# Performance work log

Hardware: AMD Instinct MI355X
Metric: run time of the kernel (lower is better)

The kernel has to match this reference:

```python
import jax, jax.numpy as jnp
import numpy as np

N, E = 50000, 800000
D_IN, D_HID, D_OUT = 128, 256, 128


def setup_inputs() -> dict:
    key = jax.random.key(0)
    k = jax.random.split(key, 7)
    x = jax.random.normal(k[0], (N, D_IN), dtype=jnp.float32)
    edge_src = jax.random.randint(k[1], (E,), 0, N, dtype=jnp.int32)
    edge_dst = jax.random.randint(k[2], (E,), 0, N, dtype=jnp.int32)
    s1 = 1.0 / np.sqrt(2 * D_IN)
    s2 = 1.0 / np.sqrt(2 * D_HID)
    W1 = jax.random.uniform(k[3], (2 * D_IN, D_HID), jnp.float32, -s1, s1)
    b1 = jax.random.uniform(k[4], (D_HID,), jnp.float32, -s1, s1)
    W2 = jax.random.uniform(k[5], (2 * D_HID, D_OUT), jnp.float32, -s2, s2)
    b2 = jax.random.uniform(k[6], (D_OUT,), jnp.float32, -s2, s2)
    return {"x": x, "edge_src": edge_src, "edge_dst": edge_dst,
            "W1": W1, "b1": b1, "W2": W2, "b2": b2}


def _sage_layer(h, edge_src, edge_dst, W, b, inv_deg):
    # mean-pool neighbor features: gather [E, D] then segment-sum to [N, D]
    msgs = h[edge_src]
    agg = jax.ops.segment_sum(msgs, edge_dst, num_segments=h.shape[0]) * inv_deg
    y = jnp.concatenate([h, agg], axis=1)  # [N, 2D]
    return y @ W + b


def reference(x, edge_src, edge_dst, W1, b1, W2, b2):
    n = x.shape[0]
    deg = jax.ops.segment_sum(jnp.ones_like(edge_dst, dtype=x.dtype), edge_dst,
                              num_segments=n)
    inv_deg = (1.0 / jnp.maximum(deg, 1.0))[:, None]  # isolated nodes -> zeros
    h = _sage_layer(x, edge_src, edge_dst, W1, b1, inv_deg)
    h = jax.nn.relu(h)
    # dropout is identity in eval mode
    h = _sage_layer(h, edge_src, edge_dst, W2, b2, inv_deg)
    return jax.nn.log_softmax(h, axis=1)
```

## Files before the change

### kernel.cpp

```cpp
#include <hip/hip_runtime.h>
#include <cstdint>
#include <cstddef>

typedef __attribute__((ext_vector_type(8))) short bf16x8;
typedef __attribute__((ext_vector_type(4))) float f32x4;
typedef __attribute__((ext_vector_type(2))) float f32x2;

__device__ inline short bf16_rne(float f) {
  unsigned u = __builtin_bit_cast(unsigned, f);
  u += 0x7fff + ((u >> 16) & 1);
  return (short)(u >> 16);
}

__device__ inline float bf16lo(unsigned v) { return __builtin_bit_cast(float, v << 16); }
__device__ inline float bf16hi(unsigned v) { return __builtin_bit_cast(float, v & 0xffff0000u); }

__device__ inline unsigned pack2(float a, float b) {
  return ((unsigned)(unsigned short)bf16_rne(a)) | (((unsigned)(unsigned short)bf16_rne(b)) << 16);
}

__device__ inline void async_copy16(const void* g, void* l) {
  __builtin_amdgcn_global_load_lds((const __attribute__((address_space(1))) void*)g,
                                   (__attribute__((address_space(3))) void*)l, 16, 0, 0);
}


__global__ __launch_bounds__(256) void bucket_hist(const int* __restrict__ dst, int E, int EPB,
                                                   int* __restrict__ histT, int SB, int NB) {
  __shared__ int h[512];
  int tid = threadIdx.x;
  for (int t = tid; t < NB; t += 256) h[t] = 0;
  __syncthreads();
  int start = blockIdx.x * EPB, end = min(E, start + EPB);
  for (int i = start + tid; i < end; i += 256) atomicAdd(&h[((unsigned)dst[i]) >> 7], 1);
  __syncthreads();
  for (int t = tid; t < NB; t += 256) histT[t * SB + blockIdx.x] = h[t];
}

__global__ __launch_bounds__(1024) void scan1_kernel(const int* __restrict__ in,
                                                     int* __restrict__ outx,
                                                     int* __restrict__ part, int n) {
  __shared__ int buf[1024];
  int tid = threadIdx.x;
  int i = blockIdx.x * 1024 + tid;
  int v = (i < n) ? in[i] : 0;
  buf[tid] = v;
  __syncthreads();
  #pragma unroll
  for (int off = 1; off < 1024; off <<= 1) {
    int t = (tid >= off) ? buf[tid - off] : 0;
    __syncthreads();
    buf[tid] += t;
    __syncthreads();
  }
  if (i < n) outx[i] = buf[tid] - v;
  if (tid == 1023) part[blockIdx.x] = buf[1023];
}

__global__ __launch_bounds__(1024) void scan2_kernel(int* __restrict__ part, int B) {
  __shared__ int buf[1024];
  int tid = threadIdx.x;
  int v = (tid < B) ? part[tid] : 0;
  buf[tid] = v;
  __syncthreads();
  #pragma unroll
  for (int off = 1; off < 1024; off <<= 1) {
    int t = (tid >= off) ? buf[tid - off] : 0;
    __syncthreads();
    buf[tid] += t;
    __syncthreads();
  }
  if (tid < B) part[tid] = buf[tid] - v;
}

__global__ __launch_bounds__(256) void bucket_scatter(const int* __restrict__ src,
                                                      const int* __restrict__ dst, int E, int EPB,
                                                      const int* __restrict__ excl,
                                                      const int* __restrict__ part, int SB, int NB,
                                                      unsigned* __restrict__ bedge) {
  __shared__ int cur[512];
  int tid = threadIdx.x;
  for (int t = tid; t < NB; t += 256) cur[t] = excl[t * SB + blockIdx.x] + part[t];
  __syncthreads();
  int start = blockIdx.x * EPB, end = min(E, start + EPB);
  for (int i = start + tid; i < end; i += 256) {
    unsigned d = (unsigned)dst[i];
    int p = atomicAdd(&cur[d >> 7], 1);
    bedge[p] = ((d & 127u) << 24) | (unsigned)src[i];
  }
}

__global__ __launch_bounds__(256) void build_csr(const unsigned* __restrict__ bedge,
                                                 const int* __restrict__ excl,
                                                 const int* __restrict__ part, int SB, int NB,
                                                 int N, int E,
                                                 int* __restrict__ offsets,
                                                 float* __restrict__ inv_deg,
                                                 int* __restrict__ ssrc) {
  __shared__ int buf[128];
  int b = blockIdx.x, tid = threadIdx.x;
  int estart = excl[b * SB] + part[b];
  int eend = (b == NB - 1) ? E : (excl[(b + 1) * SB] + part[b + 1]);
  if (tid < 128) buf[tid] = 0;
  __syncthreads();
  for (int i = estart + tid; i < eend; i += 256) atomicAdd(&buf[bedge[i] >> 24], 1);
  __syncthreads();
  int cnt = (tid < 128) ? buf[tid] : 0;
  #pragma unroll
  for (int off = 1; off < 128; off <<= 1) {
    int t = (tid >= off && tid < 128) ? buf[tid - off] : 0;
    __syncthreads();
    if (tid < 128) buf[tid] += t;
    __syncthreads();
  }
  if (tid < 128) {
    int excl_l = buf[tid] - cnt;
    int node = (b << 7) + tid;
    if (node < N) {
      offsets[node] = estart + excl_l;
      inv_deg[node] = 1.0f / fmaxf((float)cnt, 1.0f);
    }
    if (node == N) offsets[N] = E;
    buf[tid] = estart + excl_l;
  }
  __syncthreads();
  for (int i = estart + tid; i < eend; i += 256) {
    unsigned e2 = bedge[i];
    int p = atomicAdd(&buf[e2 >> 24], 1);
    ssrc[p] = (int)(e2 & 0xFFFFFFu);
  }
}

__global__ __launch_bounds__(256) void prep_kernel(const float* __restrict__ W1,
                                                   const float* __restrict__ W2,
                                                   const float* __restrict__ b2,
                                                   const float* __restrict__ x,
                                                   short* __restrict__ B1p,
                                                   short* __restrict__ B2p,
                                                   float* __restrict__ bias2,
                                                   unsigned* __restrict__ A1u,
                                                   unsigned* __restrict__ xf8, int nquads) {
  int b = blockIdx.x;
  if (b < 512) {
    int mode = b >> 8;
    int idx = (b & 255) * 256 + threadIdx.x;
    int j = idx & 7;
    int L = (idx >> 3) & 63;
    int nt = (idx >> 9) & 15;
    int kb = idx >> 13;
    int k = kb * 32 + (L >> 4) * 8 + j;
    int n = nt * 16 + (L & 15);
    if (mode == 0) {
      B1p[idx] = bf16_rne(W1[(size_t)k * 256 + n]);
    } else {
      float v = (n < 128) ? W2[(size_t)k * 128 + n] : W2[(size_t)(256 + k) * 128 + (n - 128)];
      B2p[idx] = bf16_rne(v);
    }
  } else if (b == 512) {
    int j = threadIdx.x;
    bias2[j] = (j < 128) ? b2[j] : 0.0f;
  } else {
    int idx = (b - 513) * 256 + threadIdx.x;
    if (idx < nquads) {
      int n = idx >> 5, q = idx & 31;
      float4 v = ((const float4*)x)[idx];
      ((uint2*)A1u)[(size_t)n * 64 + q] = make_uint2(pack2(v.x, v.y), pack2(v.z, v.w));
      int pk = __builtin_amdgcn_cvt_pk_fp8_f32(v.x, v.y, 0, false);
      pk = __builtin_amdgcn_cvt_pk_fp8_f32(v.z, v.w, pk, true);
      xf8[(size_t)n * 32 + q] = (unsigned)pk;
    }
  }
}


__global__ __launch_bounds__(256) void agg1_kernel(const uint2* __restrict__ X8,
                                                   const int* __restrict__ offsets,
                                                   const int* __restrict__ ssrc,
                                                   const float* __restrict__ inv_deg,
                                                   uint4* __restrict__ A1q, int N) {
  int node = blockIdx.x * 4 + (threadIdx.x >> 6);
  if (node >= N) return;
  int lane = threadIdx.x & 63;
  int g = lane >> 4;
  int l = lane & 15;
  int s = offsets[node], e = offsets[node + 1];
  float a0=0.f,a1=0.f,a2=0.f,a3=0.f,a4=0.f,a5=0.f,a6=0.f,a7=0.f;
  int i = s;
  for (; i + 8 <= e; i += 8) {
    int sA = ssrc[i + g], sB = ssrc[i + 4 + g];
    uint2 u = X8[((size_t)(unsigned)sA << 4) + l];
    uint2 v = X8[((size_t)(unsigned)sB << 4) + l];
    f32x2 p, q;
    p = __builtin_amdgcn_cvt_pk_f32_fp8(u.x, false); q = __builtin_amdgcn_cvt_pk_f32_fp8(u.x, true);
    a0 += p[0]; a1 += p[1]; a2 += q[0]; a3 += q[1];
    p = __builtin_amdgcn_cvt_pk_f32_fp8(u.y, false); q = __builtin_amdgcn_cvt_pk_f32_fp8(u.y, true);
    a4 += p[0]; a5 += p[1]; a6 += q[0]; a7 += q[1];
    p = __builtin_amdgcn_cvt_pk_f32_fp8(v.x, false); q = __builtin_amdgcn_cvt_pk_f32_fp8(v.x, true);
    a0 += p[0]; a1 += p[1]; a2 += q[0]; a3 += q[1];
    p = __builtin_amdgcn_cvt_pk_f32_fp8(v.y, false); q = __builtin_amdgcn_cvt_pk_f32_fp8(v.y, true);
    a4 += p[0]; a5 += p[1]; a6 += q[0]; a7 += q[1];
  }
  for (; i < e; i += 4) {
    if (g < e - i) {
      uint2 u = X8[((size_t)(unsigned)ssrc[i + g] << 4) + l];
      f32x2 p, q;
      p = __builtin_amdgcn_cvt_pk_f32_fp8(u.x, false); q = __builtin_amdgcn_cvt_pk_f32_fp8(u.x, true);
      a0 += p[0]; a1 += p[1]; a2 += q[0]; a3 += q[1];
      p = __builtin_amdgcn_cvt_pk_f32_fp8(u.y, false); q = __builtin_amdgcn_cvt_pk_f32_fp8(u.y, true);
      a4 += p[0]; a5 += p[1]; a6 += q[0]; a7 += q[1];
    }
  }
  a0 += __shfl_xor(a0,16,64); a0 += __shfl_xor(a0,32,64);
  a1 += __shfl_xor(a1,16,64); a1 += __shfl_xor(a1,32,64);
  a2 += __shfl_xor(a2,16,64); a2 += __shfl_xor(a2,32,64);
  a3 += __shfl_xor(a3,16,64); a3 += __shfl_xor(a3,32,64);
  a4 += __shfl_xor(a4,16,64); a4 += __shfl_xor(a4,32,64);
  a5 += __shfl_xor(a5,16,64); a5 += __shfl_xor(a5,32,64);
  a6 += __shfl_xor(a6,16,64); a6 += __shfl_xor(a6,32,64);
  a7 += __shfl_xor(a7,16,64); a7 += __shfl_xor(a7,32,64);
  if (g == 0) {
    float id = inv_deg[node];
    A1q[((size_t)node << 5) + 16 + l] =
        make_uint4(pack2(a0 * id, a1 * id), pack2(a2 * id, a3 * id),
                   pack2(a4 * id, a5 * id), pack2(a6 * id, a7 * id));
  }
}

__global__ __launch_bounds__(256) void gemm_mfma(const short* __restrict__ A,
                                                 const short* __restrict__ Bp,
                                                 const float* __restrict__ bias,
                                                 void* __restrict__ out0,
                                                 void* __restrict__ out1,
                                                 int M_pad, int mode) {
  __shared__ __align__(16) short As[4096];
  __shared__ __align__(16) short Bs[4096];
  int tid = threadIdx.x;
  int w = tid >> 6;
  int lane = tid & 63;
  int wr = w >> 1;
  int wc = w & 1;
  int bm = blockIdx.x * 128;
  int bn = blockIdx.y * 128;

  f32x4 acc[4][4];
  #pragma unroll
  for (int i = 0; i < 4; ++i)
    #pragma unroll
    for (int j = 0; j < 4; ++j) acc[i][j] = (f32x4)(0.0f);

  for (int kb = 0; kb < 8; ++kb) {
    #pragma unroll
    for (int q = 0; q < 2; ++q) {
      int f = q * 4 + w;
      int row = bm + f * 16 + (lane & 15);
      const short* g = A + (size_t)row * 256 + kb * 32 + (lane >> 4) * 8;
      async_copy16(g, &As[f * 512]);
    }
    #pragma unroll
    for (int q = 0; q < 2; ++q) {
      int f = q * 4 + w;
      const short* g = Bp + ((size_t)(kb * 16 + (bn >> 4) + f) * 64 + lane) * 8;
      async_copy16(g, &Bs[f * 512]);
    }
    __syncthreads();

    bf16x8 af[4], bfr[4];
    #pragma unroll
    for (int i = 0; i < 4; ++i)
      af[i] = *(const bf16x8*)&As[(wr * 4 + i) * 512 + lane * 8];
    #pragma unroll
    for (int j = 0; j < 4; ++j)
      bfr[j] = *(const bf16x8*)&Bs[(wc * 4 + j) * 512 + lane * 8];

    #pragma unroll
    for (int i = 0; i < 4; ++i)
      #pragma unroll
      for (int j = 0; j < 4; ++j)
        acc[i][j] = __builtin_amdgcn_mfma_f32_16x16x32_bf16(af[i], bfr[j], acc[i][j], 0, 0, 0);
    __syncthreads();
  }

  int crow0 = (lane >> 4) * 4;
  int ccol = lane & 15;
  #pragma unroll
  for (int i = 0; i < 4; ++i) {
    #pragma unroll
    for (int j = 0; j < 4; ++j) {
      int col_loc = wc * 64 + j * 16 + ccol;
      int col = bn + col_loc;
      #pragma unroll
      for (int r = 0; r < 4; ++r) {
        int row = bm + wr * 64 + i * 16 + crow0 + r;
        float v = acc[i][j][r] + bias[col];
        if (mode == 0) {
          v = fmaxf(v, 0.0f);
          ((short*)out0)[(size_t)row * 256 + col] = bf16_rne(v);
        } else if (blockIdx.y == 0) {
          ((short*)out0)[(size_t)row * 128 + col_loc] = bf16_rne(v);
        } else {
          int pk = __builtin_amdgcn_cvt_pk_fp8_f32(v, v, 0, false);
          ((unsigned char*)out1)[(size_t)row * 128 + col_loc] = (unsigned char)(pk & 0xff);
        }
      }
    }
  }
}

__global__ __launch_bounds__(256) void final_kernel(const uint4* __restrict__ utopq,
                                                    const uint2* __restrict__ T2,
                                                    const int* __restrict__ offsets,
                                                    const int* __restrict__ ssrc,
                                                    const float* __restrict__ inv_deg,
                                                    float4* __restrict__ out4, int N) {
  int node = blockIdx.x * 4 + (threadIdx.x >> 6);
  if (node >= N) return;
  int lane = threadIdx.x & 63;
  int g = lane >> 4;
  int l = lane & 15;
  int s = offsets[node], e = offsets[node + 1];
  float a0=0.f,a1=0.f,a2=0.f,a3=0.f,a4=0.f,a5=0.f,a6=0.f,a7=0.f;
  int i = s;
  for (; i + 8 <= e; i += 8) {
    int sA = ssrc[i + g], sB = ssrc[i + 4 + g];
    uint2 u = T2[((size_t)(unsigned)sA << 4) + l];
    uint2 v = T2[((size_t)(unsigned)sB << 4) + l];
    f32x2 p, q;
    p = __builtin_amdgcn_cvt_pk_f32_fp8(u.x, false); q = __builtin_amdgcn_cvt_pk_f32_fp8(u.x, true);
    a0 += p[0]; a1 += p[1]; a2 += q[0]; a3 += q[1];
    p = __builtin_amdgcn_cvt_pk_f32_fp8(u.y, false); q = __builtin_amdgcn_cvt_pk_f32_fp8(u.y, true);
    a4 += p[0]; a5 += p[1]; a6 += q[0]; a7 += q[1];
    p = __builtin_amdgcn_cvt_pk_f32_fp8(v.x, false); q = __builtin_amdgcn_cvt_pk_f32_fp8(v.x, true);
    a0 += p[0]; a1 += p[1]; a2 += q[0]; a3 += q[1];
    p = __builtin_amdgcn_cvt_pk_f32_fp8(v.y, false); q = __builtin_amdgcn_cvt_pk_f32_fp8(v.y, true);
    a4 += p[0]; a5 += p[1]; a6 += q[0]; a7 += q[1];
  }
  for (; i < e; i += 4) {
    if (g < e - i) {
      uint2 u = T2[((size_t)(unsigned)ssrc[i + g] << 4) + l];
      f32x2 p, q;
      p = __builtin_amdgcn_cvt_pk_f32_fp8(u.x, false); q = __builtin_amdgcn_cvt_pk_f32_fp8(u.x, true);
      a0 += p[0]; a1 += p[1]; a2 += q[0]; a3 += q[1];
      p = __builtin_amdgcn_cvt_pk_f32_fp8(u.y, false); q = __builtin_amdgcn_cvt_pk_f32_fp8(u.y, true);
      a4 += p[0]; a5 += p[1]; a6 += q[0]; a7 += q[1];
    }
  }
  a0 += __shfl_xor(a0,16,64); a0 += __shfl_xor(a0,32,64);
  a1 += __shfl_xor(a1,16,64); a1 += __shfl_xor(a1,32,64);
  a2 += __shfl_xor(a2,16,64); a2 += __shfl_xor(a2,32,64);
  a3 += __shfl_xor(a3,16,64); a3 += __shfl_xor(a3,32,64);
  a4 += __shfl_xor(a4,16,64); a4 += __shfl_xor(a4,32,64);
  a5 += __shfl_xor(a5,16,64); a5 += __shfl_xor(a5,32,64);
  a6 += __shfl_xor(a6,16,64); a6 += __shfl_xor(a6,32,64);
  a7 += __shfl_xor(a7,16,64); a7 += __shfl_xor(a7,32,64);
  if (g == 0) {
    float id = inv_deg[node];
    uint4 U = utopq[((size_t)node << 4) + l];
    float v0 = bf16lo(U.x) + a0 * id;
    float v1 = bf16hi(U.x) + a1 * id;
    float v2 = bf16lo(U.y) + a2 * id;
    float v3 = bf16hi(U.y) + a3 * id;
    float v4 = bf16lo(U.z) + a4 * id;
    float v5 = bf16hi(U.z) + a5 * id;
    float v6 = bf16lo(U.w) + a6 * id;
    float v7 = bf16hi(U.w) + a7 * id;
    float m = fmaxf(fmaxf(fmaxf(v0, v1), fmaxf(v2, v3)), fmaxf(fmaxf(v4, v5), fmaxf(v6, v7)));
    #pragma unroll
    for (int off = 1; off < 16; off <<= 1) m = fmaxf(m, __shfl_xor(m, off, 16));
    float su = expf(v0 - m) + expf(v1 - m) + expf(v2 - m) + expf(v3 - m) +
               expf(v4 - m) + expf(v5 - m) + expf(v6 - m) + expf(v7 - m);
    #pragma unroll
    for (int off = 1; off < 16; off <<= 1) su += __shfl_xor(su, off, 16);
    float ls = m + logf(su);
    out4[((size_t)node << 5) + l * 2]     = make_float4(v0 - ls, v1 - ls, v2 - ls, v3 - ls);
    out4[((size_t)node << 5) + l * 2 + 1] = make_float4(v4 - ls, v5 - ls, v6 - ls, v7 - ls);
  }
}

extern "C" void kernel_launch(void* const* d_in, const int* in_sizes, int n_in,
                              void* d_out, int out_size, void* d_ws, size_t ws_size,
                              hipStream_t stream) {
  const float* x        = (const float*)d_in[0];
  const int*   edge_src = (const int*)d_in[1];
  const int*   edge_dst = (const int*)d_in[2];
  const float* W1       = (const float*)d_in[3];
  const float* b1       = (const float*)d_in[4];
  const float* W2       = (const float*)d_in[5];
  const float* b2       = (const float*)d_in[6];
  float* out = (float*)d_out;

  const int D_IN = 128;
  const int N = in_sizes[0] / D_IN;
  const int E = in_sizes[1];
  const int M_pad = ((N + 127) / 128) * 128;

  const int SB = 1024;
  const int EPB = (E + SB - 1) / SB;
  const int NB = (N + 127) >> 7;
  const int M = NB * SB;
  const int sbl = (M + 1023) / 1024;

  char* ws = (char*)d_ws;
  size_t p = 0;
  auto take = [&](size_t bytes) -> size_t {
    size_t r = p;
    p += (bytes + 255) & ~(size_t)255;
    return r;
  };
  size_t histT_off = take((size_t)M * 4);
  size_t excl_off  = take((size_t)(M + 1) * 4);
  size_t part_off  = take((size_t)1024 * 4);
  size_t bedge_off = take((size_t)E * 4);
  size_t offs_off  = take((size_t)(N + 1) * 4);
  size_t inv_off   = take((size_t)N * 4);
  size_t ssrc_off  = take((size_t)E * 4);
  size_t A1_off    = take((size_t)M_pad * 256 * 2);
  size_t xf8_off   = take((size_t)M_pad * 128);
  size_t h_off     = take((size_t)M_pad * 256 * 2);
  size_t B1p_off   = take((size_t)256 * 256 * 2);
  size_t B2p_off   = take((size_t)256 * 256 * 2);
  size_t bias2_off = take((size_t)256 * 4);
  size_t utop_off  = take((size_t)M_pad * 128 * 2);
  size_t t2_off    = take((size_t)M_pad * 128);
  (void)ws_size;

  int*   histT   = (int*)(ws + histT_off);
  int*   excl    = (int*)(ws + excl_off);
  int*   part    = (int*)(ws + part_off);
  unsigned* bedge = (unsigned*)(ws + bedge_off);
  int*   offsets = (int*)(ws + offs_off);
  float* inv_deg = (float*)(ws + inv_off);
  int*   ssrc    = (int*)(ws + ssrc_off);
  unsigned* A1u  = (unsigned*)(ws + A1_off);
  unsigned* xf8  = (unsigned*)(ws + xf8_off);
  short* h       = (short*)(ws + h_off);
  short* B1p     = (short*)(ws + B1p_off);
  short* B2p     = (short*)(ws + B2p_off);
  float* bias2   = (float*)(ws + bias2_off);
  short* utop    = (short*)(ws + utop_off);
  unsigned char* t2f8 = (unsigned char*)(ws + t2_off);

  bucket_hist<<<SB, 256, 0, stream>>>(edge_dst, E, EPB, histT, SB, NB);
  scan1_kernel<<<sbl, 1024, 0, stream>>>(histT, excl, part, M);
  scan2_kernel<<<1, 1024, 0, stream>>>(part, sbl);
  bucket_scatter<<<SB, 256, 0, stream>>>(edge_src, edge_dst, E, EPB, excl, part, SB, NB, bedge);
  build_csr<<<NB, 256, 0, stream>>>(bedge, excl, part, SB, NB, N, E, offsets, inv_deg, ssrc);

  {
    int nquads = N * 32;
    int grid = 513 + (nquads + 255) / 256;
    prep_kernel<<<grid, 256, 0, stream>>>(W1, W2, b2, x, B1p, B2p, bias2, A1u, xf8, nquads);
  }

  agg1_kernel<<<(N + 3) / 4, 256, 0, stream>>>((const uint2*)xf8, offsets, ssrc, inv_deg,
                                               (uint4*)A1u, N);
  {
    dim3 grid(M_pad / 128, 2);
    gemm_mfma<<<grid, 256, 0, stream>>>((const short*)A1u, B1p, b1, h, nullptr, M_pad, 0);
  }
  {
    dim3 grid(M_pad / 128, 2);
    gemm_mfma<<<grid, 256, 0, stream>>>(h, B2p, bias2, utop, t2f8, M_pad, 1);
  }
  final_kernel<<<(N + 3) / 4, 256, 0, stream>>>((const uint4*)utop, (const uint2*)t2f8,
                                                offsets, ssrc, inv_deg, (float4*)out, N);
}
```

Before: 236.9 us.

## Fuse histogram into prep kernel, halve sort blocks, unroll gathers by sixteen

Merges the bucket histogram and the weight/feature prep work into one launch, so the independent work shares a grid and one kernel launch goes away. The sort block count drops from 1024 to 512, and the scan uses 512-thread blocks with one block per bucket. Both neighbour-aggregation kernels now gather 16 edges per iteration instead of 8, keeping more loads in flight. Fewer sort blocks means less parallelism in the scatter stage, and the deeper unroll sends more edges to the tail loop for low-degree nodes.

Result: faster. 228.6 us (-3.5%).

```diff
diff --git a/kernel.cpp b/kernel.cpp
--- a/kernel.cpp
+++ b/kernel.cpp
@@ -25,36 +25,77 @@
 }
 
 
-__global__ __launch_bounds__(256) void bucket_hist(const int* __restrict__ dst, int E, int EPB,
-                                                   int* __restrict__ histT, int SB, int NB) {
+__global__ __launch_bounds__(256) void prep_kernel(const int* __restrict__ dst, int E, int EPB,
+                                                   int* __restrict__ histT, int SB, int NB,
+                                                   const float* __restrict__ W1,
+                                                   const float* __restrict__ W2,
+                                                   const float* __restrict__ b2,
+                                                   const float* __restrict__ x,
+                                                   short* __restrict__ B1p,
+                                                   short* __restrict__ B2p,
+                                                   float* __restrict__ bias2,
+                                                   unsigned* __restrict__ A1u,
+                                                   unsigned* __restrict__ xf8, int nquads) {
   __shared__ int h[512];
+  int b = blockIdx.x;
   int tid = threadIdx.x;
-  for (int t = tid; t < NB; t += 256) h[t] = 0;
-  __syncthreads();
-  int start = blockIdx.x * EPB, end = min(E, start + EPB);
-  for (int i = start + tid; i < end; i += 256) atomicAdd(&h[((unsigned)dst[i]) >> 7], 1);
-  __syncthreads();
-  for (int t = tid; t < NB; t += 256) histT[t * SB + blockIdx.x] = h[t];
-}
-
-__global__ __launch_bounds__(1024) void scan1_kernel(const int* __restrict__ in,
-                                                     int* __restrict__ outx,
-                                                     int* __restrict__ part, int n) {
-  __shared__ int buf[1024];
+  if (b < SB) {
+    for (int t = tid; t < NB; t += 256) h[t] = 0;
+    __syncthreads();
+    int start = b * EPB, end = min(E, start + EPB);
+    for (int i = start + tid; i < end; i += 256) atomicAdd(&h[((unsigned)dst[i]) >> 7], 1);
+    __syncthreads();
+    for (int t = tid; t < NB; t += 256) histT[t * SB + b] = h[t];
+  } else if (b < SB + 512) {
+    int bb = b - SB;
+    int mode = bb >> 8;
+    int idx = (bb & 255) * 256 + tid;
+    int j = idx & 7;
+    int L = (idx >> 3) & 63;
+    int nt = (idx >> 9) & 15;
+    int kb = idx >> 13;
+    int k = kb * 32 + (L >> 4) * 8 + j;
+    int n = nt * 16 + (L & 15);
+    if (mode == 0) {
+      B1p[idx] = bf16_rne(W1[(size_t)k * 256 + n]);
+    } else {
+      float v = (n < 128) ? W2[(size_t)k * 128 + n] : W2[(size_t)(256 + k) * 128 + (n - 128)];
+      B2p[idx] = bf16_rne(v);
+    }
+  } else if (b == SB + 512) {
+    int j = tid;
+    bias2[j] = (j < 128) ? b2[j] : 0.0f;
+  } else {
+    int idx = (b - SB - 513) * 256 + tid;
+    if (idx < nquads) {
+      int n = idx >> 5, q = idx & 31;
+      float4 v = ((const float4*)x)[idx];
+      ((uint2*)A1u)[(size_t)n * 64 + q] = make_uint2(pack2(v.x, v.y), pack2(v.z, v.w));
+      int pk = __builtin_amdgcn_cvt_pk_fp8_f32(v.x, v.y, 0, false);
+      pk = __builtin_amdgcn_cvt_pk_fp8_f32(v.z, v.w, pk, true);
+      xf8[(size_t)n * 32 + q] = (unsigned)pk;
+    }
+  }
+}
+
+__global__ __launch_bounds__(512) void scan1_kernel(const int* __restrict__ in,
+                                                    int* __restrict__ outx,
+                                                    int* __restrict__ part, int n) {
+  __shared__ int buf[512];
   int tid = threadIdx.x;
-  int i = blockIdx.x * 1024 + tid;
+  int i = blockIdx.x * 512 + tid;
   int v = (i < n) ? in[i] : 0;
   buf[tid] = v;
   __syncthreads();
   #pragma unroll
-  for (int off = 1; off < 1024; off <<= 1) {
+  for (int off = 1; off < 512; off <<= 1) {
     int t = (tid >= off) ? buf[tid - off] : 0;
     __syncthreads();
     buf[tid] += t;
     __syncthreads();
   }
   if (i < n) outx[i] = buf[tid] - v;
-  if (tid == 1023) part[blockIdx.x] = buf[1023];
+  if (tid == 511) part[blockIdx.x] = buf[511];
 }
 
 __global__ __launch_bounds__(1024) void scan2_kernel(int* __restrict__ part, int B) {
@@ -131,47 +172,16 @@
   }
 }
 
-__global__ __launch_bounds__(256) void prep_kernel(const float* __restrict__ W1,
-                                                   const float* __restrict__ W2,
-                                                   const float* __restrict__ b2,
-                                                   const float* __restrict__ x,
-                                                   short* __restrict__ B1p,
-                                                   short* __restrict__ B2p,
-                                                   float* __restrict__ bias2,
-                                                   unsigned* __restrict__ A1u,
-                                                   unsigned* __restrict__ xf8, int nquads) {
-  int b = blockIdx.x;
-  if (b < 512) {
-    int mode = b >> 8;
-    int idx = (b & 255) * 256 + threadIdx.x;
-    int j = idx & 7;
-    int L = (idx >> 3) & 63;
-    int nt = (idx >> 9) & 15;
-    int kb = idx >> 13;
-    int k = kb * 32 + (L >> 4) * 8 + j;
-    int n = nt * 16 + (L & 15);
-    if (mode == 0) {
-      B1p[idx] = bf16_rne(W1[(size_t)k * 256 + n]);
-    } else {
-      float v = (n < 128) ? W2[(size_t)k * 128 + n] : W2[(size_t)(256 + k) * 128 + (n - 128)];
-      B2p[idx] = bf16_rne(v);
-    }
-  } else if (b == 512) {
-    int j = threadIdx.x;
-    bias2[j] = (j < 128) ? b2[j] : 0.0f;
-  } else {
-    int idx = (b - 513) * 256 + threadIdx.x;
-    if (idx < nquads) {
-      int n = idx >> 5, q = idx & 31;
-      float4 v = ((const float4*)x)[idx];
-      ((uint2*)A1u)[(size_t)n * 64 + q] = make_uint2(pack2(v.x, v.y), pack2(v.z, v.w));
-      int pk = __builtin_amdgcn_cvt_pk_fp8_f32(v.x, v.y, 0, false);
-      pk = __builtin_amdgcn_cvt_pk_fp8_f32(v.z, v.w, pk, true);
-      xf8[(size_t)n * 32 + q] = (unsigned)pk;
-    }
-  }
-}
-
+#define CVT8(U, A0, A1, A2, A3, A4, A5, A6, A7)                                        \
+  {                                                                                    \
+    f32x2 p_, q_;                                                                      \
+    p_ = __builtin_amdgcn_cvt_pk_f32_fp8((U).x, false);                                \
+    q_ = __builtin_amdgcn_cvt_pk_f32_fp8((U).x, true);                                 \
+    A0 += p_[0]; A1 += p_[1]; A2 += q_[0]; A3 += q_[1];                                \
+    p_ = __builtin_amdgcn_cvt_pk_f32_fp8((U).y, false);                                \
+    q_ = __builtin_amdgcn_cvt_pk_f32_fp8((U).y, true);                                 \
+    A4 += p_[0]; A5 += p_[1]; A6 += q_[0]; A7 += q_[1];                                \
+  }
 
 __global__ __launch_bounds__(256) void agg1_kernel(const uint2* __restrict__ X8,
                                                    const int* __restrict__ offsets,
@@ -186,28 +196,22 @@
   int s = offsets[node], e = offsets[node + 1];
   float a0=0.f,a1=0.f,a2=0.f,a3=0.f,a4=0.f,a5=0.f,a6=0.f,a7=0.f;
   int i = s;
-  for (; i + 8 <= e; i += 8) {
+  for (; i + 16 <= e; i += 16) {
     int sA = ssrc[i + g], sB = ssrc[i + 4 + g];
+    int sC = ssrc[i + 8 + g], sD = ssrc[i + 12 + g];
     uint2 u = X8[((size_t)(unsigned)sA << 4) + l];
     uint2 v = X8[((size_t)(unsigned)sB << 4) + l];
-    f32x2 p, q;
-    p = __builtin_amdgcn_cvt_pk_f32_fp8(u.x, false); q = __builtin_amdgcn_cvt_pk_f32_fp8(u.x, true);
-    a0 += p[0]; a1 += p[1]; a2 += q[0]; a3 += q[1];
-    p = __builtin_amdgcn_cvt_pk_f32_fp8(u.y, false); q = __builtin_amdgcn_cvt_pk_f32_fp8(u.y, true);
-    a4 += p[0]; a5 += p[1]; a6 += q[0]; a7 += q[1];
-    p = __builtin_amdgcn_cvt_pk_f32_fp8(v.x, false); q = __builtin_amdgcn_cvt_pk_f32_fp8(v.x, true);
-    a0 += p[0]; a1 += p[1]; a2 += q[0]; a3 += q[1];
-    p = __builtin_amdgcn_cvt_pk_f32_fp8(v.y, false); q = __builtin_amdgcn_cvt_pk_f32_fp8(v.y, true);
-    a4 += p[0]; a5 += p[1]; a6 += q[0]; a7 += q[1];
+    uint2 w = X8[((size_t)(unsigned)sC << 4) + l];
+    uint2 z = X8[((size_t)(unsigned)sD << 4) + l];
+    CVT8(u, a0,a1,a2,a3,a4,a5,a6,a7);
+    CVT8(v, a0,a1,a2,a3,a4,a5,a6,a7);
+    CVT8(w, a0,a1,a2,a3,a4,a5,a6,a7);
+    CVT8(z, a0,a1,a2,a3,a4,a5,a6,a7);
   }
   for (; i < e; i += 4) {
     if (g < e - i) {
       uint2 u = X8[((size_t)(unsigned)ssrc[i + g] << 4) + l];
-      f32x2 p, q;
-      p = __builtin_amdgcn_cvt_pk_f32_fp8(u.x, false); q = __builtin_amdgcn_cvt_pk_f32_fp8(u.x, true);
-      a0 += p[0]; a1 += p[1]; a2 += q[0]; a3 += q[1];
-      p = __builtin_amdgcn_cvt_pk_f32_fp8(u.y, false); q = __builtin_amdgcn_cvt_pk_f32_fp8(u.y, true);
-      a4 += p[0]; a5 += p[1]; a6 += q[0]; a7 += q[1];
+      CVT8(u, a0,a1,a2,a3,a4,a5,a6,a7);
     }
   }
   a0 += __shfl_xor(a0,16,64); a0 += __shfl_xor(a0,32,64);
@@ -320,28 +324,22 @@
   int s = offsets[node], e = offsets[node + 1];
   float a0=0.f,a1=0.f,a2=0.f,a3=0.f,a4=0.f,a5=0.f,a6=0.f,a7=0.f;
   int i = s;
-  for (; i + 8 <= e; i += 8) {
+  for (; i + 16 <= e; i += 16) {
     int sA = ssrc[i + g], sB = ssrc[i + 4 + g];
+    int sC = ssrc[i + 8 + g], sD = ssrc[i + 12 + g];
     uint2 u = T2[((size_t)(unsigned)sA << 4) + l];
     uint2 v = T2[((size_t)(unsigned)sB << 4) + l];
-    f32x2 p, q;
-    p = __builtin_amdgcn_cvt_pk_f32_fp8(u.x, false); q = __builtin_amdgcn_cvt_pk_f32_fp8(u.x, true);
-    a0 += p[0]; a1 += p[1]; a2 += q[0]; a3 += q[1];
-    p = __builtin_amdgcn_cvt_pk_f32_fp8(u.y, false); q = __builtin_amdgcn_cvt_pk_f32_fp8(u.y, true);
-    a4 += p[0]; a5 += p[1]; a6 += q[0]; a7 += q[1];
-    p = __builtin_amdgcn_cvt_pk_f32_fp8(v.x, false); q = __builtin_amdgcn_cvt_pk_f32_fp8(v.x, true);
-    a0 += p[0]; a1 += p[1]; a2 += q[0]; a3 += q[1];
-    p = __builtin_amdgcn_cvt_pk_f32_fp8(v.y, false); q = __builtin_amdgcn_cvt_pk_f32_fp8(v.y, true);
-    a4 += p[0]; a5 += p[1]; a6 += q[0]; a7 += q[1];
+    uint2 w = T2[((size_t)(unsigned)sC << 4) + l];
+    uint2 z = T2[((size_t)(unsigned)sD << 4) + l];
+    CVT8(u, a0,a1,a2,a3,a4,a5,a6,a7);
+    CVT8(v, a0,a1,a2,a3,a4,a5,a6,a7);
+    CVT8(w, a0,a1,a2,a3,a4,a5,a6,a7);
+    CVT8(z, a0,a1,a2,a3,a4,a5,a6,a7);
   }
   for (; i < e; i += 4) {
     if (g < e - i) {
       uint2 u = T2[((size_t)(unsigned)ssrc[i + g] << 4) + l];
-      f32x2 p, q;
-      p = __builtin_amdgcn_cvt_pk_f32_fp8(u.x, false); q = __builtin_amdgcn_cvt_pk_f32_fp8(u.x, true);
-      a0 += p[0]; a1 += p[1]; a2 += q[0]; a3 += q[1];
-      p = __builtin_amdgcn_cvt_pk_f32_fp8(u.y, false); q = __builtin_amdgcn_cvt_pk_f32_fp8(u.y, true);
-      a4 += p[0]; a5 += p[1]; a6 += q[0]; a7 += q[1];
+      CVT8(u, a0,a1,a2,a3,a4,a5,a6,a7);
     }
   }
   a0 += __shfl_xor(a0,16,64); a0 += __shfl_xor(a0,32,64);
@@ -393,11 +391,10 @@
   const int E = in_sizes[1];
   const int M_pad = ((N + 127) / 128) * 128;
 
-  const int SB = 1024;
+  const int SB = 512;
   const int EPB = (E + SB - 1) / SB;
   const int NB = (N + 127) >> 7;
   const int M = NB * SB;
-  const int sbl = (M + 1023) / 1024;
 
   char* ws = (char*)d_ws;
   size_t p = 0;
@@ -439,17 +436,16 @@
   short* utop    = (short*)(ws + utop_off);
   unsigned char* t2f8 = (unsigned char*)(ws + t2_off);
 
-  bucket_hist<<<SB, 256, 0, stream>>>(edge_dst, E, EPB, histT, SB, NB);
-  scan1_kernel<<<sbl, 1024, 0, stream>>>(histT, excl, part, M);
-  scan2_kernel<<<1, 1024, 0, stream>>>(part, sbl);
+  {
+    int nquads = N * 32;
+    int grid = SB + 513 + (nquads + 255) / 256;
+    prep_kernel<<<grid, 256, 0, stream>>>(edge_dst, E, EPB, histT, SB, NB,
+                                          W1, W2, b2, x, B1p, B2p, bias2, A1u, xf8, nquads);
+  }
+  scan1_kernel<<<NB, 512, 0, stream>>>(histT, excl, part, M);
+  scan2_kernel<<<1, 1024, 0, stream>>>(part, NB);
   bucket_scatter<<<SB, 256, 0, stream>>>(edge_src, edge_dst, E, EPB, excl, part, SB, NB, bedge);
   build_csr<<<NB, 256, 0, stream>>>(bedge, excl, part, SB, NB, N, E, offsets, inv_deg, ssrc);
-
-  {
-    int nquads = N * 32;
-    int grid = 513 + (nquads + 255) / 256;
-    prep_kernel<<<grid, 256, 0, stream>>>(W1, W2, b2, x, B1p, B2p, bias2, A1u, xf8, nquads);
-  }
 
   agg1_kernel<<<(N + 3) / 4, 256, 0, stream>>>((const uint2*)xf8, offsets, ssrc, inv_deg,
                                                (uint4*)A1u, N);
```
